# Kernel optimization log

Hardware: AMD Instinct MI355X
Metric: run time of the kernel (lower is better)

## Reference

```python
import jax, jax.numpy as jnp
import numpy as np

WINDOW_SIZE = 7
L = 255.0
C1 = (0.01 * L) ** 2
C2 = (0.03 * L) ** 2


def _box_filter(x, window):
    # x: [B,1,H,W], window: [1,1,k,k] (uniform 1/k^2). VALID conv, groups=1.
    return jax.lax.conv_general_dilated(
        x, window, window_strides=(1, 1), padding='VALID',
        dimension_numbers=('NCHW', 'OIHW', 'NCHW'))


def setup_inputs() -> dict:
    key = jax.random.key(0)
    k1, k2 = jax.random.split(key)
    shape = (16, 1, 1080, 1920)
    img1 = jax.random.uniform(k1, shape, dtype=jnp.float32) * L
    img2 = jax.random.uniform(k2, shape, dtype=jnp.float32) * L
    window = jnp.ones((1, 1, WINDOW_SIZE, WINDOW_SIZE), dtype=jnp.float32) / (WINDOW_SIZE * WINDOW_SIZE)
    return {"img1": img1, "img2": img2, "window": window}


def reference(img1, img2, window):
    mu1 = _box_filter(img1, window)
    mu2 = _box_filter(img2, window)
    mu1_sq = mu1 * mu1
    mu2_sq = mu2 * mu2
    mu1_mu2 = mu1 * mu2
    sigma1_sq = _box_filter(img1 * img1, window) - mu1_sq
    sigma2_sq = _box_filter(img2 * img2, window) - mu2_sq
    sigma12 = _box_filter(img1 * img2, window) - mu1_mu2
    v1 = 2.0 * sigma12 + C2
    v2 = sigma1_sq + sigma2_sq + C2
    ssim_map = (2.0 * mu1_mu2 + C1) * v1 / ((mu1_sq + mu2_sq + C1) * v2)
    return jnp.mean(ssim_map)
```

## Files before the change

kernel.cpp:

```cpp
#include <hip/hip_runtime.h>


constexpr int W_IN = 1920, H_IN = 1080;
constexpr int WOUT = W_IN - 6;
constexpr int HOUT = H_IN - 6;
constexpr int NBATCH = 16;
constexpr int WCOLS = 122;
constexpr int TW = 4 * WCOLS;
constexpr int TH = 35;
constexpr int NBX = 4, NBY = 31;
constexpr int NBLK = NBX * NBY * NBATCH;

constexpr float C1f = 6.5025f;
constexpr float C2f = 58.5225f;
constexpr float INV49 = 1.0f / 49.0f;

__device__ __forceinline__ float bperm(int addr, float v) {
  return __int_as_float(__builtin_amdgcn_ds_bpermute(addr, __float_as_int(v)));
}

__global__ __attribute__((amdgpu_flat_work_group_size(256, 256),
                          amdgpu_waves_per_eu(8, 8)))
void ssim_kernel(const float* __restrict__ img1, const float* __restrict__ img2,
                 double* __restrict__ partial) {
  __shared__ float wsum[4];

  const int t = threadIdx.x;
  const int lane = t & 63;
  const int xw = blockIdx.x * TW + (t >> 6) * WCOLS;
  const int y0 = blockIdx.y * TH;
  const size_t ib = (size_t)blockIdx.z * (size_t)(H_IN * W_IN);
  const float* __restrict__ p1 = img1 + ib;
  const float* __restrict__ p2 = img2 + ib;

  const int gcol = min(xw + 2 * lane, W_IN - 2);
  const int up1 = ((lane + 1) & 63) << 2;
  const int up2 = ((lane + 2) & 63) << 2;
  const int up3 = ((lane + 3) & 63) << 2;
  const bool lv = lane < 61;
  const bool m0 = lv && (xw + 2 * lane + 0 < WOUT);
  const bool m1 = lv && (xw + 2 * lane + 1 < WOUT);

  float V1_0 = 0.f, V1_1 = 0.f;
  float V2_0 = 0.f, V2_1 = 0.f;
  float V3_0 = 0.f, V3_1 = 0.f;
  float V4_0 = 0.f, V4_1 = 0.f;
  float V5_0 = 0.f, V5_1 = 0.f;
  float accv = 0.f;

  float2 Aa = *(const float2*)(p1 + (size_t)y0 * W_IN + gcol);
  float2 Ab = *(const float2*)(p2 + (size_t)y0 * W_IN + gcol);
  float2 Ba, Bb, Pa, Pb, Qa, Qb;
  int gyn = y0 + 1;
  int gyo = y0 + 1;
  int oy = y0;

#define EPI1(VA, VB, VAA, VBB, VAB, MASK)                                   \
  {                                                                         \
    const float mu1 = (VA) * INV49, mu2 = (VB) * INV49;                     \
    const float mu1s = mu1 * mu1, mu2s = mu2 * mu2, mu12 = mu1 * mu2;       \
    const float sg1 = fmaf((VAA), INV49, -mu1s);                            \
    const float sg2 = fmaf((VBB), INV49, -mu2s);                            \
    const float sg12 = fmaf((VAB), INV49, -mu12);                           \
    const float v1 = fmaf(2.f, sg12, C2f);                                  \
    const float v2 = sg1 + sg2 + C2f;                                       \
    const float num = fmaf(2.f, mu12, C1f) * v1;                            \
    const float den = (mu1s + mu2s + C1f) * v2;                             \
    const float ss = num * __builtin_amdgcn_rcpf(den);                      \
    accv += (MASK) ? ss : 0.f;                                              \
  }

#define HQ(Q)                                                               \
    const float s1_##Q = bperm(up1, H##Q);                                  \
    const float s2_##Q = bperm(up2, H##Q);                                  \
    const float s3_##Q = bperm(up3, H##Q);                                  \
    const float f3_##Q = bperm(up3, V##Q##_0);                              \
    const float sh_##Q = s1_##Q + s2_##Q;                                   \
    const float h0_##Q = (H##Q + sh_##Q) + f3_##Q;                          \
    const float h1_##Q = (V##Q##_1 + sh_##Q) + s3_##Q;

#define VUPD_ADD(CAa, CAb)                                                  \
    V1_0 += CAa.x;                   V1_1 += CAa.y;                         \
    V2_0 += CAb.x;                   V2_1 += CAb.y;                         \
    V3_0 = fmaf(CAa.x, CAa.x, V3_0); V3_1 = fmaf(CAa.y, CAa.y, V3_1);       \
    V4_0 = fmaf(CAb.x, CAb.x, V4_0); V4_1 = fmaf(CAb.y, CAb.y, V4_1);       \
    V5_0 = fmaf(CAa.x, CAb.x, V5_0); V5_1 = fmaf(CAa.y, CAb.y, V5_1);

#define VUPD_SUB(COa, COb)                                                  \
    V1_0 -= COa.x;                     V1_1 -= COa.y;                       \
    V2_0 -= COb.x;                     V2_1 -= COb.y;                       \
    V3_0 = fmaf(-COa.x, COa.x, V3_0);  V3_1 = fmaf(-COa.y, COa.y, V3_1);    \
    V4_0 = fmaf(-COb.x, COb.x, V4_0);  V4_1 = fmaf(-COb.y, COb.y, V4_1);    \
    V5_0 = fmaf(-COa.x, COb.x, V5_0);  V5_1 = fmaf(-COa.y, COb.y, V5_1);

#define DO_EPI_BLOCK                                                        \
    if (oy < HOUT) {                                                        \
      const float H1 = V1_0 + V1_1;                                         \
      const float H2 = V2_0 + V2_1;                                         \
      const float H3 = V3_0 + V3_1;                                         \
      const float H4 = V4_0 + V4_1;                                         \
      const float H5 = V5_0 + V5_1;                                         \
      HQ(1) HQ(2) HQ(3) HQ(4) HQ(5)                                         \
      EPI1(h0_1, h0_2, h0_3, h0_4, h0_5, m0)                                \
      EPI1(h1_1, h1_2, h1_3, h1_4, h1_5, m1)                                \
    }                                                                       \
    ++oy;

#define STEPW(CAa, CAb, NAa, NAb, DO_EPI)                                   \
  {                                                                         \
    NAa = *(const float2*)(p1 + (size_t)gyn * W_IN + gcol);                 \
    NAb = *(const float2*)(p2 + (size_t)gyn * W_IN + gcol);                 \
    gyn = min(gyn + 1, H_IN - 1);                                           \
    VUPD_ADD(CAa, CAb)                                                      \
    if (DO_EPI) { DO_EPI_BLOCK }                                            \
  }

#define STEPM(CAa, CAb, NAa, NAb, COa, COb, NOa, NOb)                       \
  {                                                                         \
    NAa = *(const float2*)(p1 + (size_t)gyn * W_IN + gcol);                 \
    NAb = *(const float2*)(p2 + (size_t)gyn * W_IN + gcol);                 \
    gyn = min(gyn + 1, H_IN - 1);                                           \
    {                                                                       \
      const int yo = min(gyo, H_IN - 1);                                    \
      NOa = *(const float2*)(p1 + (size_t)yo * W_IN + gcol);                \
      NOb = *(const float2*)(p2 + (size_t)yo * W_IN + gcol);                \
      ++gyo;                                                                \
    }                                                                       \
    VUPD_ADD(CAa, CAb)                                                      \
    VUPD_SUB(COa, COb)                                                      \
    DO_EPI_BLOCK                                                            \
  }

  STEPW(Aa, Ab, Ba, Bb, false)
  STEPW(Ba, Bb, Aa, Ab, false)
  STEPW(Aa, Ab, Ba, Bb, false)
  STEPW(Ba, Bb, Aa, Ab, false)
  STEPW(Aa, Ab, Ba, Bb, false)
  STEPW(Ba, Bb, Aa, Ab, false)
  STEPW(Aa, Ab, Ba, Bb, true)
  Pa = *(const float2*)(p1 + (size_t)y0 * W_IN + gcol);
  Pb = *(const float2*)(p2 + (size_t)y0 * W_IN + gcol);
  for (int gp = 0; gp < 17; ++gp) {
    STEPM(Ba, Bb, Aa, Ab, Pa, Pb, Qa, Qb)
    STEPM(Aa, Ab, Ba, Bb, Qa, Qb, Pa, Pb)
  }
#undef STEPM
#undef STEPW
#undef DO_EPI_BLOCK
#undef VUPD_SUB
#undef VUPD_ADD
#undef HQ
#undef EPI1

#pragma unroll
  for (int off = 32; off > 0; off >>= 1) accv += __shfl_down(accv, off);
  if ((t & 63) == 0) wsum[t >> 6] = accv;
  __syncthreads();
  if (t == 0) {
    const int bid = blockIdx.x + NBX * (blockIdx.y + NBY * blockIdx.z);
    partial[bid] = (double)wsum[0] + (double)wsum[1] +
                   (double)wsum[2] + (double)wsum[3];
  }
}

__global__ __launch_bounds__(256)
void finalize_kernel(const double* __restrict__ partial,
                     float* __restrict__ out) {
  const int tid = threadIdx.x;
  double s = 0.0;
  for (int i = tid; i < NBLK; i += 256) s += partial[i];
#pragma unroll
  for (int off = 32; off > 0; off >>= 1) s += __shfl_down(s, off);
  __shared__ double ws[4];
  if ((tid & 63) == 0) ws[tid >> 6] = s;
  __syncthreads();
  if (tid == 0) {
    const double tot = ws[0] + ws[1] + ws[2] + ws[3];
    out[0] = (float)(tot / ((double)NBATCH * (double)HOUT * (double)WOUT));
  }
}

extern "C" void kernel_launch(void* const* d_in, const int* in_sizes, int n_in,
                              void* d_out, int out_size, void* d_ws, size_t ws_size,
                              hipStream_t stream) {
  const float* img1 = (const float*)d_in[0];
  const float* img2 = (const float*)d_in[1];
  double* partial = (double*)d_ws;
  dim3 grid(NBX, NBY, NBATCH);
  hipLaunchKernelGGL(ssim_kernel, grid, dim3(256), 0, stream, img1, img2,
                     partial);
  hipLaunchKernelGGL(finalize_kernel, dim3(1), dim3(256), 0, stream, partial,
                     (float*)d_out);
}
```

Before: 294.6 us.

## Use 16-lane row segments with DPP row shifts instead of ds_bpermute

Reorganizes each wave into four 16-lane segments of 26 output columns so the horizontal window sums can use DPP row_shl instead of ds_bpermute. This removes the LDS-crossbar permute latency from the epilogue. In exchange, halo lanes now waste 3 of every 16 lanes, which adds redundant loads and arithmetic. Tile height, grid shape and the waves-per-EU hint are also changed.

```diff
diff --git a/kernel.cpp b/kernel.cpp
--- a/kernel.cpp
+++ b/kernel.cpp
@@ -5,41 +5,44 @@
 constexpr int WOUT = W_IN - 6;
 constexpr int HOUT = H_IN - 6;
 constexpr int NBATCH = 16;
-constexpr int WCOLS = 122;
-constexpr int TW = 4 * WCOLS;
-constexpr int TH = 35;
-constexpr int NBX = 4, NBY = 31;
+constexpr int RCOLS = 26;
+constexpr int TW = 16 * RCOLS;
+constexpr int TH = 43;
+constexpr int NBX = 5, NBY = 25;
 constexpr int NBLK = NBX * NBY * NBATCH;
 
 constexpr float C1f = 6.5025f;
 constexpr float C2f = 58.5225f;
 constexpr float INV49 = 1.0f / 49.0f;
 
-__device__ __forceinline__ float bperm(int addr, float v) {
-  return __int_as_float(__builtin_amdgcn_ds_bpermute(addr, __float_as_int(v)));
+template <int CTRL>
+__device__ __forceinline__ float dpp_shl(float v) {
+  return __int_as_float(__builtin_amdgcn_update_dpp(
+      0, __float_as_int(v), CTRL, 0xf, 0xf, true));
 }
+#define SHL1(v) dpp_shl<0x101>(v)
+#define SHL2(v) dpp_shl<0x102>(v)
+#define SHL3(v) dpp_shl<0x103>(v)
 
-__global__ __attribute__((amdgpu_flat_work_group_size(256, 256),
-                          amdgpu_waves_per_eu(8, 8)))
+__global__ __attribute__((amdgpu_flat_work_group_size(256, 256)))
 void ssim_kernel(const float* __restrict__ img1, const float* __restrict__ img2,
                  double* __restrict__ partial) {
   __shared__ float wsum[4];
 
   const int t = threadIdx.x;
   const int lane = t & 63;
-  const int xw = blockIdx.x * TW + (t >> 6) * WCOLS;
+  const int sub = lane & 15;
+  const int xr = blockIdx.x * TW + (t >> 4) * RCOLS;
   const int y0 = blockIdx.y * TH;
   const size_t ib = (size_t)blockIdx.z * (size_t)(H_IN * W_IN);
   const float* __restrict__ p1 = img1 + ib;
   const float* __restrict__ p2 = img2 + ib;
 
-  const int gcol = min(xw + 2 * lane, W_IN - 2);
-  const int up1 = ((lane + 1) & 63) << 2;
-  const int up2 = ((lane + 2) & 63) << 2;
-  const int up3 = ((lane + 3) & 63) << 2;
-  const bool lv = lane < 61;
-  const bool m0 = lv && (xw + 2 * lane + 0 < WOUT);
-  const bool m1 = lv && (xw + 2 * lane + 1 < WOUT);
+  const int c0 = xr + 2 * sub;
+  const int gcol = min(c0, W_IN - 2);
+  const bool pv = sub < 13;
+  const bool m0 = pv && (c0 + 0 < WOUT);
+  const bool m1 = pv && (c0 + 1 < WOUT);
 
   float V1_0 = 0.f, V1_1 = 0.f;
   float V2_0 = 0.f, V2_1 = 0.f;
@@ -71,10 +74,10 @@
   }
 
 #define HQ(Q)                                                               \
-    const float s1_##Q = bperm(up1, H##Q);                                  \
-    const float s2_##Q = bperm(up2, H##Q);                                  \
-    const float s3_##Q = bperm(up3, H##Q);                                  \
-    const float f3_##Q = bperm(up3, V##Q##_0);                              \
+    const float s1_##Q = SHL1(H##Q);                                        \
+    const float s2_##Q = SHL2(H##Q);                                        \
+    const float s3_##Q = SHL3(H##Q);                                        \
+    const float f3_##Q = SHL3(V##Q##_0);                                    \
     const float sh_##Q = s1_##Q + s2_##Q;                                   \
     const float h0_##Q = (H##Q + sh_##Q) + f3_##Q;                          \
     const float h1_##Q = (V##Q##_1 + sh_##Q) + s3_##Q;
@@ -140,7 +143,7 @@
   STEPW(Aa, Ab, Ba, Bb, true)
   Pa = *(const float2*)(p1 + (size_t)y0 * W_IN + gcol);
   Pb = *(const float2*)(p2 + (size_t)y0 * W_IN + gcol);
-  for (int gp = 0; gp < 17; ++gp) {
+  for (int gp = 0; gp < 21; ++gp) {
     STEPM(Ba, Bb, Aa, Ab, Pa, Pb, Qa, Qb)
     STEPM(Aa, Ab, Ba, Bb, Qa, Qb, Pa, Pb)
   }
```

After: 295.7 us. No clear change (+0.4%).
